# Kernel tuning notes

Measured on AMD Instinct MI355X. Metric: run time of the kernel, lower is better.

## Reference

```python
import jax, jax.numpy as jnp
import numpy as np

N = 50000       # num nodes
F_IN = 256      # num_features
HID = 128       # num_hidden
E = 800000      # structural edges (no self loops)
E_KNN = 500000  # knn edges (no self loops)


def setup_inputs() -> dict:
    rng = np.random.default_rng(0)
    # loop-free random edges: col != row guaranteed
    row = rng.integers(0, N, E)
    col = (row + 1 + rng.integers(0, N - 1, E)) % N
    edge_index = jnp.asarray(np.stack([row, col]), dtype=jnp.int32)
    rowk = rng.integers(0, N, E_KNN)
    colk = (rowk + 1 + rng.integers(0, N - 1, E_KNN)) % N
    knn_graph = jnp.asarray(np.stack([rowk, colk]), dtype=jnp.int32)

    key = jax.random.key(0)
    ks = jax.random.split(key, 8)
    x = jax.random.normal(ks[0], (N, F_IN), dtype=jnp.float32)
    s = 1.0 / np.sqrt(F_IN)  # nn.Linear default init range
    def lin(kw, kb):
        W = jax.random.uniform(kw, (HID, F_IN), minval=-s, maxval=s, dtype=jnp.float32)
        b = jax.random.uniform(kb, (HID,), minval=-s, maxval=s, dtype=jnp.float32)
        return W, b
    W_s1, b_s1 = lin(ks[1], ks[2])
    W_s2, b_s2 = lin(ks[3], ks[4])
    W_f2, b_f2 = lin(ks[5], ks[6])
    return {"x": x, "edge_index": edge_index, "knn_graph": knn_graph,
            "W_s1": W_s1, "b_s1": b_s1, "W_s2": W_s2, "b_s2": b_s2,
            "W_f2": W_f2, "b_f2": b_f2}


def _gcn_norm(edge_index, num_nodes):
    # add_remaining_self_loops on loop-free input == append all self loops (w=1)
    loop = jnp.arange(num_nodes, dtype=edge_index.dtype)
    row = jnp.concatenate([edge_index[0], loop])
    col = jnp.concatenate([edge_index[1], loop])
    w = jnp.ones(row.shape[0], dtype=jnp.float32)
    deg = jax.ops.segment_sum(w, col, num_segments=num_nodes)
    dinv = jnp.where(deg > 0, jax.lax.rsqrt(deg), 0.0)
    return row, col, dinv[row] * w * dinv[col]


def _gcn(x, W, b, row, col, norm, K):
    # eval mode: dropout(p=0.6) is identity
    h = x @ W.T + b
    n = x.shape[0]
    for _ in range(K):
        # gather source feats -> edge-weight scale -> scatter-add to targets (SpMM)
        h = jax.ops.segment_sum(norm[:, None] * h[row], col, num_segments=n)
    return h


def reference(x, edge_index, knn_graph, W_s1, b_s1, W_s2, b_s2, W_f2, b_f2):
    n = x.shape[0]
    r, c, nm = _gcn_norm(edge_index, n)
    rk, ck, nmk = _gcn_norm(knn_graph, n)
    h0 = _gcn(x, W_s1, b_s1, r, c, nm, 2)
    h1 = _gcn(x, W_s2, b_s2, r, c, nm, 10)
    z0 = _gcn(x, W_f2, b_f2, r, c, nm, 2)
    # original computes gcn_f2(x, edge_index, K=2) twice; in eval mode both equal z0
    z1 = z0 + _gcn(x, W_f2, b_f2, rk, ck, nmk, 1)
    return (h0, h1, z0, z1)
```

## Files before the change

kernel.cpp:

```cpp
#include <hip/hip_runtime.h>
#include <hip/hip_fp16.h>

#define F_IN 256
#define HID 128

typedef _Float16 half8 __attribute__((ext_vector_type(8)));
typedef _Float16 half4v __attribute__((ext_vector_type(4)));
typedef float f32x4 __attribute__((ext_vector_type(4)));
typedef unsigned int uint4v __attribute__((ext_vector_type(4)));


__global__ void k_count_cvt(const int* __restrict__ col_s, int E, int* __restrict__ cnt_s,
                            const int* __restrict__ col_k, int EK, int* __restrict__ cnt_k,
                            int nbE,
                            const float* __restrict__ W0, const float* __restrict__ W1,
                            const float* __restrict__ W2, _Float16* __restrict__ Wh) {
  if ((int)blockIdx.x < nbE) {
    int e = blockIdx.x * 256 + threadIdx.x;
    if (e < E) {
      atomicAdd(&cnt_s[col_s[e]], 1);
    } else {
      int f = e - E;
      if (f < EK) atomicAdd(&cnt_k[col_k[f]], 1);
    }
  } else {
    const int sz = HID * F_IN;
    int idx = ((blockIdx.x - nbE) * 256 + threadIdx.x) * 4;
    const float* src = (idx < sz) ? (W0 + idx)
                     : (idx < 2 * sz) ? (W1 + idx - sz)
                     : (W2 + idx - 2 * sz);
    float4 v = *(const float4*)src;
    half4v o;
    o[0] = (_Float16)v.x; o[1] = (_Float16)v.y; o[2] = (_Float16)v.z; o[3] = (_Float16)v.w;
    *(half4v*)(Wh + idx) = o;
  }
}

__global__ void k_scan_block2(const int* __restrict__ in0, const int* __restrict__ in1,
                              int n, int* __restrict__ out0, int* __restrict__ out1,
                              int* __restrict__ bsum) {
  const int* in = blockIdx.y ? in1 : in0;
  int* out = blockIdx.y ? out1 : out0;
  int* bs = bsum + blockIdx.y * 512;
  __shared__ int s[1024];
  int tid = threadIdx.x;
  int i = blockIdx.x * 1024 + tid;
  int v = (i < n) ? in[i] : 0;
  s[tid] = v;
  __syncthreads();
  for (int off = 1; off < 1024; off <<= 1) {
    int t = (tid >= off) ? s[tid - off] : 0;
    __syncthreads();
    s[tid] += t;
    __syncthreads();
  }
  if (i < n) out[i] = s[tid] - v;
  if (tid == 1023) bs[blockIdx.x] = s[1023];
}

__global__ void k_scan_single2(int* __restrict__ bsum, int nb,
                               int* __restrict__ tail0, int* __restrict__ tail1) {
  if (threadIdx.x == 0 && blockIdx.x == 0) {
    int run = 0;
    for (int b = 0; b < nb; ++b) { int t = bsum[b]; bsum[b] = run; run += t; }
    *tail0 = run;
    run = 0;
    for (int b = 0; b < nb; ++b) { int t = bsum[512 + b]; bsum[512 + b] = run; run += t; }
    *tail1 = run;
  }
}

__global__ void k_add_off2(int* __restrict__ out0, int* __restrict__ out1,
                           const int* __restrict__ bsum, int n) {
  int* out = blockIdx.y ? out1 : out0;
  const int* bs = bsum + blockIdx.y * 512;
  int i = blockIdx.x * blockDim.x + threadIdx.x;
  if (i < n) out[i] += bs[i >> 10];
}


__device__ inline half8 cvt8(float4 a, float4 b) {
  half8 v;
  v[0] = (_Float16)a.x; v[1] = (_Float16)a.y; v[2] = (_Float16)a.z; v[3] = (_Float16)a.w;
  v[4] = (_Float16)b.x; v[5] = (_Float16)b.y; v[6] = (_Float16)b.z; v[7] = (_Float16)b.w;
  return v;
}

__global__ __launch_bounds__(256, 3) void k_gemm3_scatter(
    const float* __restrict__ x, const _Float16* __restrict__ Wh,
    const float* __restrict__ b0, const float* __restrict__ b1, const float* __restrict__ b2,
    int n, const int* __restrict__ cnt_s, const int* __restrict__ cnt_k,
    _Float16* __restrict__ gS1, _Float16* __restrict__ gS2,
    _Float16* __restrict__ gF2s, _Float16* __restrict__ gF2k,
    const int* __restrict__ row_s, const int* __restrict__ col_s, int E,
    const int* __restrict__ offs_s, int* __restrict__ cur_s, int* __restrict__ csr_s,
    const int* __restrict__ row_k, const int* __restrict__ col_k, int EK,
    const int* __restrict__ offs_k, int* __restrict__ cur_k, int* __restrict__ csr_k,
    int nbG)
{
  __shared__ __align__(16) char lds[49152];
  int tid = threadIdx.x;

  if ((int)blockIdx.x >= nbG) {
    int e = (blockIdx.x - nbG) * 256 + tid;
    if (e < E) {
      int c = col_s[e];
      int p = offs_s[c] + atomicAdd(&cur_s[c], 1);
      csr_s[p] = row_s[e];
    } else {
      int f = e - E;
      if (f < EK) {
        int c = col_k[f];
        int p = offs_k[c] + atomicAdd(&cur_k[c], 1);
        csr_k[p] = row_k[f];
      }
    }
    return;
  }

  int m0 = blockIdx.x * 64;

  int rA = tid >> 2;
  int cA0 = (tid & 3) * 2, cA1 = cA0 + 1;
  int gnA = m0 + rA; if (gnA >= n) gnA = n - 1;
  const float* xA = x + (size_t)gnA * F_IN;
  unsigned aw0 = (unsigned)(rA * 128 + ((cA0 ^ (rA & 7)) << 4));
  unsigned aw1 = (unsigned)(rA * 128 + ((cA1 ^ (rA & 7)) << 4));
  int rB = tid >> 1;
  int cB0 = (tid & 1) * 4;
  unsigned bw[4];
#pragma unroll
  for (int i = 0; i < 4; ++i)
    bw[i] = (unsigned)(rB * 128 + (((cB0 + i) ^ (rB & 7)) << 4));

  int lane = tid & 63;
  int wv = tid >> 6;
  int wm = wv >> 1, wn = wv & 1;
  int l15 = lane & 15, lhi = lane >> 4;
  unsigned koff0 = (unsigned)(((0 * 4 + lhi) ^ (l15 & 7)) << 4);
  unsigned koff1 = (unsigned)(((1 * 4 + lhi) ^ (l15 & 7)) << 4);
  unsigned raw0 = (unsigned)((wm * 32 + 0 * 16 + l15) * 128);
  unsigned raw1 = (unsigned)((wm * 32 + 1 * 16 + l15) * 128);
  unsigned rbw[4];
#pragma unroll
  for (int ni = 0; ni < 4; ++ni)
    rbw[ni] = (unsigned)((wn * 64 + ni * 16 + l15) * 128);

  int nodebase = m0 + wm * 32 + l15;
  float ss[2], sk[2];
#pragma unroll
  for (int mi = 0; mi < 2; ++mi) {
    int nd = nodebase + mi * 16;
    int cn = (nd < n) ? nd : (n - 1);
    ss[mi] = rsqrtf((float)(cnt_s[cn] + 1));
    sk[mi] = rsqrtf((float)(cnt_k[cn] + 1));
  }

#pragma unroll 1
  for (int w = 0; w < 3; ++w) {
    const float* bias = (w == 0) ? b0 : (w == 1) ? b1 : b2;
    _Float16* dst = (w == 0) ? gS1 : (w == 1) ? gS2 : gF2s;
    const _Float16* WB = Wh + (size_t)w * (HID * F_IN) + (size_t)rB * F_IN;

    f32x4 acc[2][4];
#pragma unroll
    for (int ni = 0; ni < 4; ++ni) {
      float4 bv = *(const float4*)(bias + wn * 64 + ni * 16 + lhi * 4);
      f32x4 b4 = {bv.x, bv.y, bv.z, bv.w};
      acc[0][ni] = b4; acc[1][ni] = b4;
    }

    float4 fa[4]; uint4v ub[4];
    fa[0] = *(const float4*)(xA + 0 * 64 + cA0 * 8);
    fa[1] = *(const float4*)(xA + 0 * 64 + cA0 * 8 + 4);
    fa[2] = *(const float4*)(xA + 0 * 64 + cA1 * 8);
    fa[3] = *(const float4*)(xA + 0 * 64 + cA1 * 8 + 4);
#pragma unroll
    for (int i = 0; i < 4; ++i)
      ub[i] = *(const uint4v*)(WB + 0 * 64 + (cB0 + i) * 8);

#pragma unroll
    for (int kt = 0; kt < 4; ++kt) {
      char* Ab = lds + (kt & 1) * 8192;
      char* Bb = lds + 16384 + (kt & 1) * 16384;
      *(half8*)(Ab + aw0) = cvt8(fa[0], fa[1]);
      *(half8*)(Ab + aw1) = cvt8(fa[2], fa[3]);
#pragma unroll
      for (int i = 0; i < 4; ++i) *(uint4v*)(Bb + bw[i]) = ub[i];
      if (kt < 3) {
        fa[0] = *(const float4*)(xA + (kt + 1) * 64 + cA0 * 8);
        fa[1] = *(const float4*)(xA + (kt + 1) * 64 + cA0 * 8 + 4);
        fa[2] = *(const float4*)(xA + (kt + 1) * 64 + cA1 * 8);
        fa[3] = *(const float4*)(xA + (kt + 1) * 64 + cA1 * 8 + 4);
#pragma unroll
        for (int i = 0; i < 4; ++i)
          ub[i] = *(const uint4v*)(WB + (kt + 1) * 64 + (cB0 + i) * 8);
      }
      __syncthreads();
      {
        const char* Ar = Ab; const char* Br = Bb;
#pragma unroll
        for (int ks = 0; ks < 2; ++ks) {
          unsigned ko = ks ? koff1 : koff0;
          half8 xf0 = *(const half8*)(Ar + raw0 + ko);
          half8 xf1 = *(const half8*)(Ar + raw1 + ko);
          half8 wf0 = *(const half8*)(Br + rbw[0] + ko);
          half8 wf1 = *(const half8*)(Br + rbw[1] + ko);
          half8 wf2 = *(const half8*)(Br + rbw[2] + ko);
          half8 wf3 = *(const half8*)(Br + rbw[3] + ko);
          acc[0][0] = __builtin_amdgcn_mfma_f32_16x16x32_f16(wf0, xf0, acc[0][0], 0, 0, 0);
          acc[0][1] = __builtin_amdgcn_mfma_f32_16x16x32_f16(wf1, xf0, acc[0][1], 0, 0, 0);
          acc[0][2] = __builtin_amdgcn_mfma_f32_16x16x32_f16(wf2, xf0, acc[0][2], 0, 0, 0);
          acc[0][3] = __builtin_amdgcn_mfma_f32_16x16x32_f16(wf3, xf0, acc[0][3], 0, 0, 0);
          acc[1][0] = __builtin_amdgcn_mfma_f32_16x16x32_f16(wf0, xf1, acc[1][0], 0, 0, 0);
          acc[1][1] = __builtin_amdgcn_mfma_f32_16x16x32_f16(wf1, xf1, acc[1][1], 0, 0, 0);
          acc[1][2] = __builtin_amdgcn_mfma_f32_16x16x32_f16(wf2, xf1, acc[1][2], 0, 0, 0);
          acc[1][3] = __builtin_amdgcn_mfma_f32_16x16x32_f16(wf3, xf1, acc[1][3], 0, 0, 0);
        }
      }
    }

#pragma unroll
    for (int mi = 0; mi < 2; ++mi) {
      int nd = nodebase + mi * 16;
      if (nd < n) {
        size_t ob = (size_t)nd * HID + wn * 64 + lhi * 4;
        float s1 = ss[mi];
#pragma unroll
        for (int ni = 0; ni < 4; ++ni) {
          half4v o;
          o[0] = (_Float16)(acc[mi][ni][0] * s1); o[1] = (_Float16)(acc[mi][ni][1] * s1);
          o[2] = (_Float16)(acc[mi][ni][2] * s1); o[3] = (_Float16)(acc[mi][ni][3] * s1);
          *(half4v*)(dst + ob + ni * 16) = o;
        }
        if (w == 2) {
          float s2 = sk[mi];
#pragma unroll
          for (int ni = 0; ni < 4; ++ni) {
            half4v o2;
            o2[0] = (_Float16)(acc[mi][ni][0] * s2); o2[1] = (_Float16)(acc[mi][ni][1] * s2);
            o2[2] = (_Float16)(acc[mi][ni][2] * s2); o2[3] = (_Float16)(acc[mi][ni][3] * s2);
            *(half4v*)(gF2k + ob + ni * 16) = o2;
          }
        }
      }
    }
  }
}


__device__ inline float2 h2f2(unsigned int u) {
  __half2 h; *(unsigned int*)&h = u; return __half22float2(h);
}

__device__ __forceinline__ void spmm_body(
    const _Float16* gin, void* gout,
    const int* csr, const int* offs, const int* cnt,
    int n, int mode, const float* addsrc, int bid)
{
  int w = (bid << 2) | ((int)threadIdx.x >> 6);
  if (w >= n) return;
  int lane = threadIdx.x & 63;
  int g = lane >> 4;
  int c = lane & 15;
  int beg = offs[w], end = offs[w + 1];

  float acc[8];
#pragma unroll
  for (int i = 0; i < 8; ++i) acc[i] = 0.f;

  int e = beg;
#pragma unroll 1
  for (; e + 16 <= end; e += 16) {
    int idx[4];
#pragma unroll
    for (int j = 0; j < 4; ++j) idx[j] = csr[e + 4 * j + g];
    uint4v u[4];
#pragma unroll
    for (int j = 0; j < 4; ++j)
      u[j] = *(const uint4v*)(gin + ((size_t)(unsigned)idx[j] << 7) + c * 8);
#pragma unroll
    for (int j = 0; j < 4; ++j)
#pragma unroll
      for (int q = 0; q < 4; ++q) {
        float2 v = h2f2(u[j][q]);
        acc[q * 2] += v.x; acc[q * 2 + 1] += v.y;
      }
  }
#pragma unroll 1
  for (; e + 4 <= end; e += 4) {
    int idx = csr[e + g];
    uint4v u = *(const uint4v*)(gin + ((size_t)(unsigned)idx << 7) + c * 8);
#pragma unroll
    for (int q = 0; q < 4; ++q) {
      float2 v = h2f2(u[q]);
      acc[q * 2] += v.x; acc[q * 2 + 1] += v.y;
    }
  }
  {
    int rem = end - e;
    if (g < rem) {
      int idx = csr[e + g];
      uint4v u = *(const uint4v*)(gin + ((size_t)(unsigned)idx << 7) + c * 8);
#pragma unroll
      for (int q = 0; q < 4; ++q) {
        float2 v = h2f2(u[q]);
        acc[q * 2] += v.x; acc[q * 2 + 1] += v.y;
      }
    }
  }
#pragma unroll
  for (int i = 0; i < 8; ++i) {
    acc[i] += __shfl_xor(acc[i], 16, 64);
    acc[i] += __shfl_xor(acc[i], 32, 64);
  }
  {
    uint4v u = *(const uint4v*)(gin + ((size_t)w << 7) + c * 8);
#pragma unroll
    for (int q = 0; q < 4; ++q) {
      float2 v = h2f2(u[q]);
      acc[q * 2] += v.x; acc[q * 2 + 1] += v.y;
    }
  }

  float deg = (float)(cnt[w] + 1);
  if (mode == 0) {
    float sc = 1.0f / deg;
    if (g == 0) {
      uint4v o;
#pragma unroll
      for (int q = 0; q < 4; ++q) {
        __half2 h = __float22half2_rn(make_float2(acc[q * 2] * sc, acc[q * 2 + 1] * sc));
        o[q] = *(unsigned int*)&h;
      }
      *(uint4v*)((_Float16*)gout + ((size_t)w << 7) + c * 8) = o;
    }
  } else {
    float sc = rsqrtf(deg);
    if (g == 0) {
      float o[8];
#pragma unroll
      for (int i = 0; i < 8; ++i) o[i] = acc[i] * sc;
      if (mode == 2) {
        const float* ap = addsrc + ((size_t)w << 7) + c * 8;
        float4 a0 = *(const float4*)ap;
        float4 a1 = *(const float4*)(ap + 4);
        o[0] += a0.x; o[1] += a0.y; o[2] += a0.z; o[3] += a0.w;
        o[4] += a1.x; o[5] += a1.y; o[6] += a1.z; o[7] += a1.w;
      }
      float* op = (float*)gout + ((size_t)w << 7) + c * 8;
      *(float4*)op = make_float4(o[0], o[1], o[2], o[3]);
      *(float4*)(op + 4) = make_float4(o[4], o[5], o[6], o[7]);
    }
  }
}

__global__ __launch_bounds__(256) void k_spmm_h(
    const _Float16* __restrict__ gin, void* __restrict__ gout,
    const int* __restrict__ csr, const int* __restrict__ offs, const int* __restrict__ cnt,
    int n, int mode, const float* __restrict__ addsrc)
{
  spmm_body(gin, gout, csr, offs, cnt, n, mode, addsrc, blockIdx.x);
}

__global__ __launch_bounds__(256) void k_spmm_dual(
    const _Float16* ginA, void* goutA,
    const int* csrA, const int* offsA, const int* cntA, int modeA, const float* addA,
    const _Float16* ginB, void* goutB,
    const int* csrB, const int* offsB, const int* cntB, int modeB, const float* addB,
    int nblkA, int n)
{
  if ((int)blockIdx.x < nblkA) {
    spmm_body(ginA, goutA, csrA, offsA, cntA, n, modeA, addA, blockIdx.x);
  } else {
    spmm_body(ginB, goutB, csrB, offsB, cntB, n, modeB, addB, blockIdx.x - nblkA);
  }
}

__global__ __launch_bounds__(256) void k_spmm3(
    const _Float16* __restrict__ g0, const _Float16* __restrict__ g1,
    const _Float16* __restrict__ g2,
    void* __restrict__ o0, void* __restrict__ o1, void* __restrict__ o2,
    int md0, int md1, int md2,
    const int* __restrict__ csr, const int* __restrict__ offs, const int* __restrict__ cnt,
    int n)
{
  int w = (blockIdx.x << 2) | ((int)threadIdx.x >> 6);
  if (w >= n) return;
  int lane = threadIdx.x & 63;
  int g = lane >> 4;
  int c = lane & 15;
  int beg = offs[w], end = offs[w + 1];

  float a0[8], a1[8], a2[8];
#pragma unroll
  for (int i = 0; i < 8; ++i) { a0[i] = 0.f; a1[i] = 0.f; a2[i] = 0.f; }

  int e = beg;
#pragma unroll 1
  for (; e + 4 <= end; e += 4) {
    size_t off = ((size_t)(unsigned)csr[e + g] << 7) + c * 8;
    uint4v u0 = *(const uint4v*)(g0 + off);
    uint4v u1 = *(const uint4v*)(g1 + off);
    uint4v u2 = *(const uint4v*)(g2 + off);
#pragma unroll
    for (int q = 0; q < 4; ++q) {
      float2 v;
      v = h2f2(u0[q]); a0[q * 2] += v.x; a0[q * 2 + 1] += v.y;
      v = h2f2(u1[q]); a1[q * 2] += v.x; a1[q * 2 + 1] += v.y;
      v = h2f2(u2[q]); a2[q * 2] += v.x; a2[q * 2 + 1] += v.y;
    }
  }
  {
    int rem = end - e;
    if (g < rem) {
      size_t off = ((size_t)(unsigned)csr[e + g] << 7) + c * 8;
      uint4v u0 = *(const uint4v*)(g0 + off);
      uint4v u1 = *(const uint4v*)(g1 + off);
      uint4v u2 = *(const uint4v*)(g2 + off);
#pragma unroll
      for (int q = 0; q < 4; ++q) {
        float2 v;
        v = h2f2(u0[q]); a0[q * 2] += v.x; a0[q * 2 + 1] += v.y;
        v = h2f2(u1[q]); a1[q * 2] += v.x; a1[q * 2 + 1] += v.y;
        v = h2f2(u2[q]); a2[q * 2] += v.x; a2[q * 2 + 1] += v.y;
      }
    }
  }
#pragma unroll
  for (int i = 0; i < 8; ++i) {
    a0[i] += __shfl_xor(a0[i], 16, 64); a0[i] += __shfl_xor(a0[i], 32, 64);
    a1[i] += __shfl_xor(a1[i], 16, 64); a1[i] += __shfl_xor(a1[i], 32, 64);
    a2[i] += __shfl_xor(a2[i], 16, 64); a2[i] += __shfl_xor(a2[i], 32, 64);
  }
  {
    size_t off = ((size_t)w << 7) + c * 8;
    uint4v u0 = *(const uint4v*)(g0 + off);
    uint4v u1 = *(const uint4v*)(g1 + off);
    uint4v u2 = *(const uint4v*)(g2 + off);
#pragma unroll
    for (int q = 0; q < 4; ++q) {
      float2 v;
      v = h2f2(u0[q]); a0[q * 2] += v.x; a0[q * 2 + 1] += v.y;
      v = h2f2(u1[q]); a1[q * 2] += v.x; a1[q * 2 + 1] += v.y;
      v = h2f2(u2[q]); a2[q * 2] += v.x; a2[q * 2 + 1] += v.y;
    }
  }

  float deg = (float)(cnt[w] + 1);
  if (g == 0) {
    float inv = 1.0f / deg, rs = rsqrtf(deg);
    {
      float sc = (md0 == 0) ? inv : rs;
      if (md0 == 0) {
        uint4v o;
#pragma unroll
        for (int q = 0; q < 4; ++q) {
          __half2 h = __float22half2_rn(make_float2(a0[q * 2] * sc, a0[q * 2 + 1] * sc));
          o[q] = *(unsigned int*)&h;
        }
        *(uint4v*)((_Float16*)o0 + ((size_t)w << 7) + c * 8) = o;
      } else {
        float* op = (float*)o0 + ((size_t)w << 7) + c * 8;
        *(float4*)op = make_float4(a0[0] * sc, a0[1] * sc, a0[2] * sc, a0[3] * sc);
        *(float4*)(op + 4) = make_float4(a0[4] * sc, a0[5] * sc, a0[6] * sc, a0[7] * sc);
      }
    }
    {
      float sc = (md1 == 0) ? inv : rs;
      if (md1 == 0) {
        uint4v o;
#pragma unroll
        for (int q = 0; q < 4; ++q) {
          __half2 h = __float22half2_rn(make_float2(a1[q * 2] * sc, a1[q * 2 + 1] * sc));
          o[q] = *(unsigned int*)&h;
        }
        *(uint4v*)((_Float16*)o1 + ((size_t)w << 7) + c * 8) = o;
      } else {
        float* op = (float*)o1 + ((size_t)w << 7) + c * 8;
        *(float4*)op = make_float4(a1[0] * sc, a1[1] * sc, a1[2] * sc, a1[3] * sc);
        *(float4*)(op + 4) = make_float4(a1[4] * sc, a1[5] * sc, a1[6] * sc, a1[7] * sc);
      }
    }
    {
      float sc = (md2 == 0) ? inv : rs;
      if (md2 == 0) {
        uint4v o;
#pragma unroll
        for (int q = 0; q < 4; ++q) {
          __half2 h = __float22half2_rn(make_float2(a2[q * 2] * sc, a2[q * 2 + 1] * sc));
          o[q] = *(unsigned int*)&h;
        }
        *(uint4v*)((_Float16*)o2 + ((size_t)w << 7) + c * 8) = o;
      } else {
        float* op = (float*)o2 + ((size_t)w << 7) + c * 8;
        *(float4*)op = make_float4(a2[0] * sc, a2[1] * sc, a2[2] * sc, a2[3] * sc);
        *(float4*)(op + 4) = make_float4(a2[4] * sc, a2[5] * sc, a2[6] * sc, a2[7] * sc);
      }
    }
  }
}


extern "C" void kernel_launch(void* const* d_in, const int* in_sizes, int n_in,
                              void* d_out, int out_size, void* d_ws, size_t ws_size,
                              hipStream_t stream) {
  const float* x    = (const float*)d_in[0];
  const int*   ei   = (const int*)d_in[1];
  const int*   knn  = (const int*)d_in[2];
  const float* W_s1 = (const float*)d_in[3];
  const float* b_s1 = (const float*)d_in[4];
  const float* W_s2 = (const float*)d_in[5];
  const float* b_s2 = (const float*)d_in[6];
  const float* W_f2 = (const float*)d_in[7];
  const float* b_f2 = (const float*)d_in[8];

  const int N  = in_sizes[0] / F_IN;
  const int E  = in_sizes[1] / 2;
  const int EK = in_sizes[2] / 2;
  const int* row_s = ei;   const int* col_s = ei + E;
  const int* row_k = knn;  const int* col_k = knn + EK;

  char* p = (char*)d_ws;
  auto carve = [&](size_t bytes) {
    char* r = p; p += (bytes + 511) & ~(size_t)511; return (void*)r;
  };
  int* cnt_s = (int*)carve((size_t)N * 4);
  int* cnt_k = (int*)carve((size_t)N * 4);
  int* cur_s = (int*)carve((size_t)N * 4);
  int* cur_k = (int*)carve((size_t)N * 4);
  char* zero_end = p;
  int* offs_s = (int*)carve((size_t)(N + 1) * 4);
  int* offs_k = (int*)carve((size_t)(N + 1) * 4);
  int* bsum   = (int*)carve(4096);
  int* csr_s  = (int*)carve((size_t)E * 4);
  int* csr_k  = (int*)carve((size_t)EK * 4);
  _Float16* Wh  = (_Float16*)carve((size_t)3 * HID * F_IN * 2);
  _Float16* gS1 = (_Float16*)carve((size_t)N * HID * 2);
  _Float16* gS2 = (_Float16*)carve((size_t)N * HID * 2);
  _Float16* gF2s= (_Float16*)carve((size_t)N * HID * 2);
  _Float16* gF2k= (_Float16*)carve((size_t)N * HID * 2);
  _Float16* tS2 = (_Float16*)carve((size_t)N * HID * 2);

  float* out_h0 = (float*)d_out;
  float* out_h1 = out_h0 + (size_t)N * HID;
  float* out_z0 = out_h1 + (size_t)N * HID;
  float* out_z1 = out_z0 + (size_t)N * HID;
  _Float16* tS1 = (_Float16*)out_z1;
  _Float16* tF2 = tS1 + (size_t)N * HID;

  hipMemsetAsync(d_ws, 0, (size_t)(zero_end - (char*)d_ws), stream);

  const int tpb = 256;
  int etot = E + EK;
  int nbE = (etot + tpb - 1) / tpb;
  k_count_cvt<<<nbE + 96, tpb, 0, stream>>>(col_s, E, cnt_s, col_k, EK, cnt_k, nbE,
                                            W_s1, W_s2, W_f2, Wh);

  int nb = (N + 1023) / 1024;
  dim3 sg(nb, 2);
  k_scan_block2<<<sg, 1024, 0, stream>>>(cnt_s, cnt_k, N, offs_s, offs_k, bsum);
  k_scan_single2<<<1, 64, 0, stream>>>(bsum, nb, offs_s + N, offs_k + N);
  dim3 ag((N + tpb - 1) / tpb, 2);
  k_add_off2<<<ag, tpb, 0, stream>>>(offs_s, offs_k, bsum, N);

  int nbG = (N + 63) / 64;
  k_gemm3_scatter<<<nbG + nbE, 256, 0, stream>>>(
      x, Wh, b_s1, b_s2, b_f2, N, cnt_s, cnt_k, gS1, gS2, gF2s, gF2k,
      row_s, col_s, E, offs_s, cur_s, csr_s,
      row_k, col_k, EK, offs_k, cur_k, csr_k, nbG);

  int spmm_grid = (N + 3) / 4;

  k_spmm3<<<spmm_grid, 256, 0, stream>>>(gS1, gS2, gF2s,
                                         tS1, tS2, tF2, 0, 0, 0,
                                         csr_s, offs_s, cnt_s, N);
  k_spmm3<<<spmm_grid, 256, 0, stream>>>(tS1, tS2, tF2,
                                         out_h0, gS1, out_z0, 1, 0, 1,
                                         csr_s, offs_s, cnt_s, N);

  k_spmm_dual<<<spmm_grid * 2, 256, 0, stream>>>(
      gS1, tS2, csr_s, offs_s, cnt_s, 0, nullptr,
      gF2k, out_z1, csr_k, offs_k, cnt_k, 2, out_z0,
      spmm_grid, N);

  {
    _Float16* cur = tS2; _Float16* alt = gS1;
    for (int it = 0; it < 6; ++it) {
      k_spmm_h<<<spmm_grid, 256, 0, stream>>>(cur, alt,
                                              csr_s, offs_s, cnt_s, N, 0, nullptr);
      _Float16* t = cur; cur = alt; alt = t;
    }
    k_spmm_h<<<spmm_grid, 256, 0, stream>>>(cur, out_h1,
                                            csr_s, offs_s, cnt_s, N, 1, nullptr);
  }
}
```

Baseline: 628.7 us.

## Keep x tile resident in LDS across all three weight GEMMs with 32-row tiles

The GEMM part of the fused gemm+scatter kernel now loads and converts each block's x rows to fp16 once into LDS, as a full 256-wide K slab, and reuses it for all three weight matrices instead of reloading x per weight. The tile shrinks from 64 to 32 nodes per block, LDS drops to 32 KB and launch bounds rise to 5 blocks per CU for higher occupancy. A single B buffer is used, with weight loads prefetched across kt and w boundaries and a barrier before each B write. The smaller tile halves weight reuse per block and doubles the GEMM grid, and single-buffering adds sync points.

```diff
diff --git a/kernel.cpp b/kernel.cpp
--- a/kernel.cpp
+++ b/kernel.cpp
@@ -86,7 +86,7 @@
   return v;
 }
 
-__global__ __launch_bounds__(256, 3) void k_gemm3_scatter(
+__global__ __launch_bounds__(256, 5) void k_gemm3_scatter(
     const float* __restrict__ x, const _Float16* __restrict__ Wh,
     const float* __restrict__ b0, const float* __restrict__ b1, const float* __restrict__ b2,
     int n, const int* __restrict__ cnt_s, const int* __restrict__ cnt_k,
@@ -98,7 +98,7 @@
     const int* __restrict__ offs_k, int* __restrict__ cur_k, int* __restrict__ csr_k,
     int nbG)
 {
-  __shared__ __align__(16) char lds[49152];
+  __shared__ __align__(16) char lds[32768];
   int tid = threadIdx.x;
 
   if ((int)blockIdx.x >= nbG) {
@@ -118,130 +118,120 @@
     return;
   }
 
-  int m0 = blockIdx.x * 64;
-
-  int rA = tid >> 2;
-  int cA0 = (tid & 3) * 2, cA1 = cA0 + 1;
-  int gnA = m0 + rA; if (gnA >= n) gnA = n - 1;
-  const float* xA = x + (size_t)gnA * F_IN;
-  unsigned aw0 = (unsigned)(rA * 128 + ((cA0 ^ (rA & 7)) << 4));
-  unsigned aw1 = (unsigned)(rA * 128 + ((cA1 ^ (rA & 7)) << 4));
-  int rB = tid >> 1;
-  int cB0 = (tid & 1) * 4;
-  unsigned bw[4];
+  int m0 = blockIdx.x * 32;
+
+  {
+    int rA = tid >> 3;
+    int cA = (tid & 7) * 4;
+    int gnA = m0 + rA; if (gnA >= n) gnA = n - 1;
+    const float* src = x + (size_t)gnA * F_IN;
+    char* drow = (char*)lds + rA * 512;
+    unsigned sw = (unsigned)(rA & 7);
+#pragma unroll
+    for (int i = 0; i < 4; ++i) {
+      int ch = cA + i;
+      float4 a = *(const float4*)(src + ch * 8);
+      float4 b = *(const float4*)(src + ch * 8 + 4);
+      *(half8*)(drow + (((unsigned)ch ^ sw) << 4)) = cvt8(a, b);
+    }
+  }
+
+  int colB = tid >> 1;
+  int hB = (tid & 1) * 4;
+  char* Bl = (char*)lds + 16384;
+  unsigned swB = (unsigned)(colB & 7);
+  unsigned bwadr[4];
 #pragma unroll
   for (int i = 0; i < 4; ++i)
-    bw[i] = (unsigned)(rB * 128 + (((cB0 + i) ^ (rB & 7)) << 4));
+    bwadr[i] = (unsigned)(colB * 128) + ((((unsigned)(hB + i)) ^ swB) << 4);
+  const _Float16* WBbase = Wh + (size_t)colB * F_IN + hB * 8;
 
   int lane = tid & 63;
   int wv = tid >> 6;
   int wm = wv >> 1, wn = wv & 1;
   int l15 = lane & 15, lhi = lane >> 4;
-  unsigned koff0 = (unsigned)(((0 * 4 + lhi) ^ (l15 & 7)) << 4);
-  unsigned koff1 = (unsigned)(((1 * 4 + lhi) ^ (l15 & 7)) << 4);
-  unsigned raw0 = (unsigned)((wm * 32 + 0 * 16 + l15) * 128);
-  unsigned raw1 = (unsigned)((wm * 32 + 1 * 16 + l15) * 128);
-  unsigned rbw[4];
-#pragma unroll
-  for (int ni = 0; ni < 4; ++ni)
-    rbw[ni] = (unsigned)((wn * 64 + ni * 16 + l15) * 128);
-
-  int nodebase = m0 + wm * 32 + l15;
-  float ss[2], sk[2];
-#pragma unroll
-  for (int mi = 0; mi < 2; ++mi) {
-    int nd = nodebase + mi * 16;
-    int cn = (nd < n) ? nd : (n - 1);
-    ss[mi] = rsqrtf((float)(cnt_s[cn] + 1));
-    sk[mi] = rsqrtf((float)(cnt_k[cn] + 1));
-  }
+  int arow = wm * 16 + l15;
+  const char* Arow = (const char*)lds + arow * 512;
+  unsigned swA = (unsigned)(arow & 7);
+  unsigned rbadr[4];
+#pragma unroll
+  for (int ni = 0; ni < 4; ++ni) {
+    int col = wn * 64 + ni * 16 + l15;
+    rbadr[ni] = 16384u + (unsigned)(col * 128);
+  }
+  unsigned rbsw = (unsigned)((wn * 64 + l15) & 7);
+
+  int node = m0 + arow;
+  int cn = (node < n) ? node : (n - 1);
+  float ss = rsqrtf((float)(cnt_s[cn] + 1));
+  float sk = rsqrtf((float)(cnt_k[cn] + 1));
+
+  uint4v ub[4];
+#pragma unroll
+  for (int i = 0; i < 4; ++i)
+    ub[i] = *(const uint4v*)(WBbase + i * 8);
 
 #pragma unroll 1
   for (int w = 0; w < 3; ++w) {
     const float* bias = (w == 0) ? b0 : (w == 1) ? b1 : b2;
     _Float16* dst = (w == 0) ? gS1 : (w == 1) ? gS2 : gF2s;
-    const _Float16* WB = Wh + (size_t)w * (HID * F_IN) + (size_t)rB * F_IN;
-
-    f32x4 acc[2][4];
+
+    f32x4 acc[4];
 #pragma unroll
     for (int ni = 0; ni < 4; ++ni) {
       float4 bv = *(const float4*)(bias + wn * 64 + ni * 16 + lhi * 4);
-      f32x4 b4 = {bv.x, bv.y, bv.z, bv.w};
-      acc[0][ni] = b4; acc[1][ni] = b4;
-    }
-
-    float4 fa[4]; uint4v ub[4];
-    fa[0] = *(const float4*)(xA + 0 * 64 + cA0 * 8);
-    fa[1] = *(const float4*)(xA + 0 * 64 + cA0 * 8 + 4);
-    fa[2] = *(const float4*)(xA + 0 * 64 + cA1 * 8);
-    fa[3] = *(const float4*)(xA + 0 * 64 + cA1 * 8 + 4);
-#pragma unroll
-    for (int i = 0; i < 4; ++i)
-      ub[i] = *(const uint4v*)(WB + 0 * 64 + (cB0 + i) * 8);
+      acc[ni] = (f32x4){bv.x, bv.y, bv.z, bv.w};
+    }
 
 #pragma unroll
     for (int kt = 0; kt < 4; ++kt) {
-      char* Ab = lds + (kt & 1) * 8192;
-      char* Bb = lds + 16384 + (kt & 1) * 16384;
-      *(half8*)(Ab + aw0) = cvt8(fa[0], fa[1]);
-      *(half8*)(Ab + aw1) = cvt8(fa[2], fa[3]);
-#pragma unroll
-      for (int i = 0; i < 4; ++i) *(uint4v*)(Bb + bw[i]) = ub[i];
-      if (kt < 3) {
-        fa[0] = *(const float4*)(xA + (kt + 1) * 64 + cA0 * 8);
-        fa[1] = *(const float4*)(xA + (kt + 1) * 64 + cA0 * 8 + 4);
-        fa[2] = *(const float4*)(xA + (kt + 1) * 64 + cA1 * 8);
-        fa[3] = *(const float4*)(xA + (kt + 1) * 64 + cA1 * 8 + 4);
-#pragma unroll
-        for (int i = 0; i < 4; ++i)
-          ub[i] = *(const uint4v*)(WB + (kt + 1) * 64 + (cB0 + i) * 8);
+      if (!(w == 0 && kt == 0)) __syncthreads();
+#pragma unroll
+      for (int i = 0; i < 4; ++i) *(uint4v*)(Bl + bwadr[i]) = ub[i];
+      {
+        int nw = (kt < 3) ? w : w + 1;
+        int nk = (kt < 3) ? kt + 1 : 0;
+        if (nw < 3) {
+          const _Float16* s = WBbase + (size_t)nw * (HID * F_IN) + nk * 64;
+#pragma unroll
+          for (int i = 0; i < 4; ++i)
+            ub[i] = *(const uint4v*)(s + i * 8);
+        }
       }
       __syncthreads();
-      {
-        const char* Ar = Ab; const char* Br = Bb;
-#pragma unroll
-        for (int ks = 0; ks < 2; ++ks) {
-          unsigned ko = ks ? koff1 : koff0;
-          half8 xf0 = *(const half8*)(Ar + raw0 + ko);
-          half8 xf1 = *(const half8*)(Ar + raw1 + ko);
-          half8 wf0 = *(const half8*)(Br + rbw[0] + ko);
-          half8 wf1 = *(const half8*)(Br + rbw[1] + ko);
-          half8 wf2 = *(const half8*)(Br + rbw[2] + ko);
-          half8 wf3 = *(const half8*)(Br + rbw[3] + ko);
-          acc[0][0] = __builtin_amdgcn_mfma_f32_16x16x32_f16(wf0, xf0, acc[0][0], 0, 0, 0);
-          acc[0][1] = __builtin_amdgcn_mfma_f32_16x16x32_f16(wf1, xf0, acc[0][1], 0, 0, 0);
-          acc[0][2] = __builtin_amdgcn_mfma_f32_16x16x32_f16(wf2, xf0, acc[0][2], 0, 0, 0);
-          acc[0][3] = __builtin_amdgcn_mfma_f32_16x16x32_f16(wf3, xf0, acc[0][3], 0, 0, 0);
-          acc[1][0] = __builtin_amdgcn_mfma_f32_16x16x32_f16(wf0, xf1, acc[1][0], 0, 0, 0);
-          acc[1][1] = __builtin_amdgcn_mfma_f32_16x16x32_f16(wf1, xf1, acc[1][1], 0, 0, 0);
-          acc[1][2] = __builtin_amdgcn_mfma_f32_16x16x32_f16(wf2, xf1, acc[1][2], 0, 0, 0);
-          acc[1][3] = __builtin_amdgcn_mfma_f32_16x16x32_f16(wf3, xf1, acc[1][3], 0, 0, 0);
-        }
-      }
-    }
-
-#pragma unroll
-    for (int mi = 0; mi < 2; ++mi) {
-      int nd = nodebase + mi * 16;
-      if (nd < n) {
-        size_t ob = (size_t)nd * HID + wn * 64 + lhi * 4;
-        float s1 = ss[mi];
+#pragma unroll
+      for (int ks = 0; ks < 2; ++ks) {
+        unsigned ach = (unsigned)(kt * 8 + ks * 4 + lhi);
+        half8 xf = *(const half8*)(Arow + ((ach ^ swA) << 4));
+        unsigned bch = (unsigned)(ks * 4 + lhi);
+        unsigned bo = ((bch ^ rbsw) << 4);
+        half8 wf0 = *(const half8*)((const char*)lds + rbadr[0] + bo);
+        half8 wf1 = *(const half8*)((const char*)lds + rbadr[1] + bo);
+        half8 wf2 = *(const half8*)((const char*)lds + rbadr[2] + bo);
+        half8 wf3 = *(const half8*)((const char*)lds + rbadr[3] + bo);
+        acc[0] = __builtin_amdgcn_mfma_f32_16x16x32_f16(wf0, xf, acc[0], 0, 0, 0);
+        acc[1] = __builtin_amdgcn_mfma_f32_16x16x32_f16(wf1, xf, acc[1], 0, 0, 0);
+        acc[2] = __builtin_amdgcn_mfma_f32_16x16x32_f16(wf2, xf, acc[2], 0, 0, 0);
+        acc[3] = __builtin_amdgcn_mfma_f32_16x16x32_f16(wf3, xf, acc[3], 0, 0, 0);
+      }
+    }
+
+    if (node < n) {
+      size_t ob = (size_t)node * HID + wn * 64 + lhi * 4;
+#pragma unroll
+      for (int ni = 0; ni < 4; ++ni) {
+        half4v o;
+        o[0] = (_Float16)(acc[ni][0] * ss); o[1] = (_Float16)(acc[ni][1] * ss);
+        o[2] = (_Float16)(acc[ni][2] * ss); o[3] = (_Float16)(acc[ni][3] * ss);
+        *(half4v*)(dst + ob + ni * 16) = o;
+      }
+      if (w == 2) {
 #pragma unroll
         for (int ni = 0; ni < 4; ++ni) {
-          half4v o;
-          o[0] = (_Float16)(acc[mi][ni][0] * s1); o[1] = (_Float16)(acc[mi][ni][1] * s1);
-          o[2] = (_Float16)(acc[mi][ni][2] * s1); o[3] = (_Float16)(acc[mi][ni][3] * s1);
-          *(half4v*)(dst + ob + ni * 16) = o;
-        }
-        if (w == 2) {
-          float s2 = sk[mi];
-#pragma unroll
-          for (int ni = 0; ni < 4; ++ni) {
-            half4v o2;
-            o2[0] = (_Float16)(acc[mi][ni][0] * s2); o2[1] = (_Float16)(acc[mi][ni][1] * s2);
-            o2[2] = (_Float16)(acc[mi][ni][2] * s2); o2[3] = (_Float16)(acc[mi][ni][3] * s2);
-            *(half4v*)(gF2k + ob + ni * 16) = o2;
-          }
+          half4v o2;
+          o2[0] = (_Float16)(acc[ni][0] * sk); o2[1] = (_Float16)(acc[ni][1] * sk);
+          o2[2] = (_Float16)(acc[ni][2] * sk); o2[3] = (_Float16)(acc[ni][3] * sk);
+          *(half4v*)(gF2k + ob + ni * 16) = o2;
         }
       }
     }
@@ -564,7 +554,7 @@
   dim3 ag((N + tpb - 1) / tpb, 2);
   k_add_off2<<<ag, tpb, 0, stream>>>(offs_s, offs_k, bsum, N);
 
-  int nbG = (N + 63) / 64;
+  int nbG = (N + 31) / 32;
   k_gemm3_scatter<<<nbG + nbE, 256, 0, stream>>>(
       x, Wh, b_s1, b_s2, b_f2, N, cnt_s, cnt_k, gS1, gS2, gF2s, gF2k,
       row_s, col_s, E, offs_s, cur_s, csr_s,
```

After: 633.8 us. Within noise of the previous version (+0.8%).
